# Optimization experiments

Hardware: AMD Instinct MI355X
Metric: run time of the kernel (lower is better)

The kernel has to match this reference:

```python
import jax, jax.numpy as jnp
import numpy as np

N, E, F, H, A, C, NC, L, AH = 50000, 800000, 768, 256, 128, 128, 7, 2, 4

def _ln(x, g, b):
    m = jnp.mean(x, axis=-1, keepdims=True)
    v = jnp.var(x, axis=-1, keepdims=True)
    return (x - m) / jnp.sqrt(v + 1e-5) * g + b

def setup_inputs() -> dict:
    key = jax.random.key(0)
    ks = jax.random.split(key, 32)
    s = 0.02
    d = {}
    d['x'] = jax.random.normal(ks[0], (N, F), jnp.float32)
    d['edge_index'] = jax.random.randint(ks[1], (2, E), 0, N, jnp.int32)
    d['W_in'] = jax.random.normal(ks[2], (F, H), jnp.float32) * s
    d['b_in'] = jnp.zeros((H,), jnp.float32)
    d['gin_W1'] = jax.random.normal(ks[3], (L, H, H), jnp.float32) * s
    d['gin_b1'] = jnp.zeros((L, H), jnp.float32)
    d['gin_lng'] = jnp.ones((L, H), jnp.float32)
    d['gin_lnb'] = jnp.zeros((L, H), jnp.float32)
    d['gin_W2'] = jax.random.normal(ks[4], (L, H, H), jnp.float32) * s
    d['gin_b2'] = jnp.zeros((L, H), jnp.float32)
    d['eps'] = jnp.zeros((L,), jnp.float32)
    d['ln_g'] = jnp.ones((L, H), jnp.float32)
    d['ln_b'] = jnp.zeros((L, H), jnp.float32)
    d['att_W1'] = jax.random.normal(ks[5], (AH, H, A), jnp.float32) * s
    d['att_b1'] = jnp.zeros((AH, A), jnp.float32)
    d['att_W2'] = jax.random.normal(ks[6], (AH, A), jnp.float32) * s
    d['att_b2'] = jnp.zeros((AH,), jnp.float32)
    d['Wc1'] = jax.random.normal(ks[7], (H, C), jnp.float32) * s
    d['bc1'] = jnp.zeros((C,), jnp.float32)
    d['lnc1_g'] = jnp.ones((C,), jnp.float32)
    d['lnc1_b'] = jnp.zeros((C,), jnp.float32)
    d['Wc2'] = jax.random.normal(ks[8], (C, C // 2), jnp.float32) * s
    d['bc2'] = jnp.zeros((C // 2,), jnp.float32)
    d['lnc2_g'] = jnp.ones((C // 2,), jnp.float32)
    d['lnc2_b'] = jnp.zeros((C // 2,), jnp.float32)
    d['Wc3'] = jax.random.normal(ks[9], (C // 2, NC), jnp.float32) * s
    d['bc3'] = jnp.zeros((NC,), jnp.float32)
    return d

def reference(x, edge_index, W_in, b_in, gin_W1, gin_b1, gin_lng, gin_lnb, gin_W2, gin_b2, eps, ln_g, ln_b, att_W1, att_b1, att_W2, att_b2, Wc1, bc1, lnc1_g, lnc1_b, Wc2, bc2, lnc2_g, lnc2_b, Wc3, bc3):
    src, dst = edge_index[0], edge_index[1]
    # input projection (use_residual and input_dim != gnn_hidden)
    h = x @ W_in + b_in  # [N,H]
    for i in range(L):
        agg = jax.ops.segment_sum(h[src], dst, num_segments=N)  # GIN sum aggregation
        m = (1.0 + eps[i]) * h + agg
        m = _ln(m @ gin_W1[i] + gin_b1[i], gin_lng[i], gin_lnb[i])
        m = jax.nn.relu(m) @ gin_W2[i] + gin_b2[i]
        hn = jax.nn.relu(_ln(m, ln_g[i], ln_b[i]))
        h = hn + h  # residual (shapes match)
    # multi-head attention pooling, softmax over node dim
    s = jnp.tanh(jnp.einsum('nd,kda->kna', h, att_W1) + att_b1[:, None, :])  # [AH,N,A]
    logits = jnp.einsum('kna,ka->kn', s, att_W2) + att_b2[:, None]  # [AH,N]
    a = jax.nn.softmax(logits, axis=1)  # [AH,N]
    z = jnp.einsum('kn,nd->kd', a, h)  # [AH,H]
    z_agg = jnp.mean(z, axis=0)  # [H]
    attn = a.T  # [N,AH]
    # classifier (full variant)
    c = jax.nn.relu(_ln(z_agg @ Wc1 + bc1, lnc1_g, lnc1_b))
    c = jax.nn.relu(_ln(c @ Wc2 + bc2, lnc2_g, lnc2_b))
    probs = jax.nn.softmax(c @ Wc3 + bc3, axis=0)
    return probs, attn
```

## Files before the change

kernel.cpp:

```cpp
#include <hip/hip_runtime.h>
#include <math.h>

#define NN 50000
#define NE 800000
#define FF 768
#define HH 256

typedef __attribute__((ext_vector_type(8))) short short8;
typedef __attribute__((ext_vector_type(4))) float f32x4;

__device__ inline unsigned short f2bf(float f) {
  unsigned u = __float_as_uint(f);
  u = u + 0x7fffu + ((u >> 16) & 1u);
  return (unsigned short)(u >> 16);
}
__device__ inline float bf2f(unsigned short b) {
  return __uint_as_float(((unsigned)b) << 16);
}

__device__ __forceinline__ void ldsload16(const unsigned short* g, unsigned short* l) {
  __builtin_amdgcn_global_load_lds(
      (const __attribute__((address_space(1))) void*)g,
      (__attribute__((address_space(3))) void*)l, 16, 0, 0);
}

__global__ void k_count(const int* __restrict__ dstv, int* __restrict__ deg) {
  int e = blockIdx.x * 256 + threadIdx.x;
  if (e < NE) atomicAdd(&deg[dstv[e]], 1);
}

__global__ void k_scan(const int* __restrict__ deg, int* __restrict__ rowptr) {
  const int CH = 49;
  int tid = threadIdx.x;
  int lane = tid & 63, w = tid >> 6;
  int base = tid * CH;
  int sum = 0;
  for (int i = 0; i < CH; i++) {
    int idx = base + i;
    if (idx < NN) sum += deg[idx];
  }
  int incl = sum;
  for (int off = 1; off < 64; off <<= 1) {
    int tv = __shfl_up(incl, off, 64);
    if (lane >= off) incl += tv;
  }
  __shared__ int ws[16];
  if (lane == 63) ws[w] = incl;
  __syncthreads();
  if (tid == 0) {
    int c = 0;
    for (int i = 0; i < 16; i++) { int tv = ws[i]; ws[i] = c; c += tv; }
  }
  __syncthreads();
  int run = ws[w] + (incl - sum);
  if (tid == 0) rowptr[0] = 0;
  for (int i = 0; i < CH; i++) {
    int idx = base + i;
    if (idx < NN) { run += deg[idx]; rowptr[idx + 1] = run; }
  }
}

__global__ void k_scatter(const int* __restrict__ srcv, const int* __restrict__ dstv,
                          int* __restrict__ cursor, int* __restrict__ csr_src) {
  int e = blockIdx.x * 256 + threadIdx.x;
  if (e < NE) {
    int d = dstv[e];
    int pos = atomicAdd(&cursor[d], 1);
    csr_src[pos] = srcv[e];
  }
}

__global__ void k_agg(const unsigned short* __restrict__ hb, const int* __restrict__ rowptr,
                      const int* __restrict__ csr_src, const float* __restrict__ eps,
                      int layer, unsigned short* __restrict__ mb) {
  int node = (blockIdx.x * blockDim.x + threadIdx.x) >> 6;
  int lane = threadIdx.x & 63;
  if (node >= NN) return;
  int beg = rowptr[node], end = rowptr[node + 1];
  const ushort4* hv = (const ushort4*)hb;
  float ax = 0.f, ay = 0.f, az = 0.f, aw = 0.f;
  for (int e = beg; e < end; ++e) {
    int s = csr_src[e];
    ushort4 v = hv[(size_t)s * 64 + lane];
    ax += bf2f(v.x); ay += bf2f(v.y); az += bf2f(v.z); aw += bf2f(v.w);
  }
  float ep = 1.0f + eps[layer];
  ushort4 h0 = hv[(size_t)node * 64 + lane];
  ax += ep * bf2f(h0.x); ay += ep * bf2f(h0.y);
  az += ep * bf2f(h0.z); aw += ep * bf2f(h0.w);
  ushort4 o;
  o.x = f2bf(ax); o.y = f2bf(ay); o.z = f2bf(az); o.w = f2bf(aw);
  *(ushort4*)&mb[(size_t)node * 256 + lane * 4] = o;
}

__global__ void k_tcast(const float* __restrict__ src0, unsigned short* __restrict__ dst0,
                        int R, int C) {
  const float* src = src0 + (size_t)blockIdx.z * R * C;
  unsigned short* dst = dst0 + (size_t)blockIdx.z * R * C;
  __shared__ float tile[32][33];
  int bx = blockIdx.x * 32, by = blockIdx.y * 32;
  int tx = threadIdx.x & 31, ty = threadIdx.x >> 5;
  for (int i = 0; i < 32; i += 8) {
    int r = by + ty + i, c = bx + tx;
    tile[ty + i][tx] = (r < R && c < C) ? src[(size_t)r * C + c] : 0.f;
  }
  __syncthreads();
  for (int i = 0; i < 32; i += 8) {
    int c = bx + ty + i, r = by + tx;
    if (c < C && r < R) dst[(size_t)c * R + r] = f2bf(tile[tx][ty + i]);
  }
}

__global__ __launch_bounds__(256) void k_mmff(
    const float* __restrict__ x, const unsigned short* __restrict__ Bt,
    const float* __restrict__ bias, float* __restrict__ outf,
    unsigned short* __restrict__ outb) {
  __shared__ unsigned short As[64 * 32];
  __shared__ unsigned short Bs[256 * 32];
  int t = threadIdx.x, lane = t & 63, wave = t >> 6;
  int row0 = blockIdx.x * 64;
  f32x4 acc[4][4];
#pragma unroll
  for (int i = 0; i < 4; i++)
#pragma unroll
    for (int j = 0; j < 4; j++) acc[i][j] = (f32x4)(0.f);
  int m16 = lane & 15, kq = lane >> 4;
  int arow = t >> 2, a2 = t & 3;
  int asl = a2 ^ (arow & 3);
  int agr = row0 + arow; if (agr >= NN) agr = NN - 1;
  int brow_[4], bsl_[4];
#pragma unroll
  for (int j = 0; j < 4; j++) {
    int s = j * 256 + t;
    brow_[j] = s >> 2;
    bsl_[j] = (s & 3) ^ (brow_[j] & 3);
  }
  for (int k0 = 0; k0 < FF; k0 += 32) {
    {
      const float* Af = x + (size_t)agr * FF + k0 + asl * 8;
      float4 f0 = *(const float4*)Af;
      float4 f1 = *(const float4*)(Af + 4);
      short8 v;
      v[0] = (short)f2bf(f0.x); v[1] = (short)f2bf(f0.y);
      v[2] = (short)f2bf(f0.z); v[3] = (short)f2bf(f0.w);
      v[4] = (short)f2bf(f1.x); v[5] = (short)f2bf(f1.y);
      v[6] = (short)f2bf(f1.z); v[7] = (short)f2bf(f1.w);
      *(short8*)&As[arow * 32 + a2 * 8] = v;
    }
#pragma unroll
    for (int j = 0; j < 4; j++)
      ldsload16(&Bt[(size_t)brow_[j] * FF + k0 + bsl_[j] * 8],
                &Bs[(j * 256 + wave * 64) * 8]);
    __syncthreads();
    short8 a[4], b[4];
#pragma unroll
    for (int rt = 0; rt < 4; rt++) {
      int row = rt * 16 + m16;
      a[rt] = *(const short8*)&As[row * 32 + ((kq ^ (row & 3)) * 8)];
    }
#pragma unroll
    for (int ct = 0; ct < 4; ct++) {
      int row = wave * 64 + ct * 16 + m16;
      b[ct] = *(const short8*)&Bs[row * 32 + ((kq ^ (row & 3)) * 8)];
    }
#pragma unroll
    for (int rt = 0; rt < 4; rt++)
#pragma unroll
      for (int ct = 0; ct < 4; ct++)
        acc[rt][ct] = __builtin_amdgcn_mfma_f32_16x16x32_bf16(a[rt], b[ct], acc[rt][ct], 0, 0, 0);
    __syncthreads();
  }
  int colbase = wave * 64 + m16;
  float bv[4];
#pragma unroll
  for (int ct = 0; ct < 4; ct++) bv[ct] = bias[colbase + ct * 16];
#pragma unroll
  for (int rt = 0; rt < 4; rt++)
#pragma unroll
    for (int reg = 0; reg < 4; reg++) {
      int r = row0 + rt * 16 + kq * 4 + reg;
      if (r < NN) {
#pragma unroll
        for (int ct = 0; ct < 4; ct++) {
          float v = acc[rt][ct][reg] + bv[ct];
          outf[(size_t)r * 256 + colbase + ct * 16] = v;
          outb[(size_t)r * 256 + colbase + ct * 16] = f2bf(v);
        }
      }
    }
}

template <bool WF>
__global__ __launch_bounds__(256) void k_gin(
    const unsigned short* __restrict__ Ab,
    const unsigned short* __restrict__ B1t, const float* __restrict__ bias1,
    const float* __restrict__ g1v, const float* __restrict__ be1,
    const unsigned short* __restrict__ B2t, const float* __restrict__ bias2,
    const float* __restrict__ g2v, const float* __restrict__ be2,
    const float* __restrict__ resid, float* __restrict__ outf,
    unsigned short* __restrict__ outb) {
  __shared__ unsigned short As[2][64 * 32];
  __shared__ unsigned short Bs[2][256 * 32];
  __shared__ unsigned short T1[64 * 256];
  __shared__ float redS[4][64];
  __shared__ float redQ[4][64];
  __shared__ float mvM[64], mvI[64];
  int t = threadIdx.x, lane = t & 63, wave = t >> 6;
  int row0 = blockIdx.x * 64;
  int m16 = lane & 15, kq = lane >> 4;
  int colbase = wave * 64 + m16;
  int arow = t >> 2, a2 = t & 3;
  int asl = a2 ^ (arow & 3);
  int agr = row0 + arow; if (agr >= NN) agr = NN - 1;
  const unsigned short* Ag = Ab + (size_t)agr * 256 + asl * 8;
  int brow_[4], bsl_[4];
#pragma unroll
  for (int j = 0; j < 4; j++) {
    int s = j * 256 + t;
    brow_[j] = s >> 2;
    bsl_[j] = (s & 3) ^ (brow_[j] & 3);
  }
  auto stage1 = [&](int c, int p) {
    int k0 = c * 32;
    ldsload16(Ag + k0, &As[p][wave * 512]);
#pragma unroll
    for (int j = 0; j < 4; j++)
      ldsload16(&B1t[(size_t)brow_[j] * 256 + k0 + bsl_[j] * 8],
                &Bs[p][(j * 256 + wave * 64) * 8]);
  };
  auto stage2 = [&](int c, int p) {
    int k0 = c * 32;
#pragma unroll
    for (int j = 0; j < 4; j++)
      ldsload16(&B2t[(size_t)brow_[j] * 256 + k0 + bsl_[j] * 8],
                &Bs[p][(j * 256 + wave * 64) * 8]);
  };

  f32x4 acc[4][4];
#pragma unroll
  for (int i = 0; i < 4; i++)
#pragma unroll
    for (int j = 0; j < 4; j++) acc[i][j] = (f32x4)(0.f);

  stage1(0, 0);
  stage1(1, 1);
#pragma unroll
  for (int c = 0; c < 8; c++) {
    if (c < 7) asm volatile("s_waitcnt vmcnt(5)" ::: "memory");
    else       asm volatile("s_waitcnt vmcnt(0)" ::: "memory");
    __builtin_amdgcn_s_barrier();
    asm volatile("" ::: "memory");
    const unsigned short* Ap = As[c & 1];
    const unsigned short* Bp = Bs[c & 1];
    short8 a[4], b[4];
#pragma unroll
    for (int rt = 0; rt < 4; rt++) {
      int row = rt * 16 + m16;
      a[rt] = *(const short8*)&Ap[row * 32 + ((kq ^ (row & 3)) * 8)];
    }
#pragma unroll
    for (int ct = 0; ct < 4; ct++) {
      int row = wave * 64 + ct * 16 + m16;
      b[ct] = *(const short8*)&Bp[row * 32 + ((kq ^ (row & 3)) * 8)];
    }
#pragma unroll
    for (int rt = 0; rt < 4; rt++)
#pragma unroll
      for (int ct = 0; ct < 4; ct++)
        acc[rt][ct] = __builtin_amdgcn_mfma_f32_16x16x32_bf16(a[rt], b[ct], acc[rt][ct], 0, 0, 0);
    asm volatile("" ::: "memory");
    __builtin_amdgcn_s_barrier();
    asm volatile("" ::: "memory");
    if (c + 2 < 8) stage1(c + 2, c & 1);
  }

  {
    float bv[4];
#pragma unroll
    for (int ct = 0; ct < 4; ct++) bv[ct] = bias1[colbase + ct * 16];
    float s[4][4], q[4][4];
#pragma unroll
    for (int rt = 0; rt < 4; rt++)
#pragma unroll
      for (int reg = 0; reg < 4; reg++) { s[rt][reg] = 0.f; q[rt][reg] = 0.f; }
#pragma unroll
    for (int rt = 0; rt < 4; rt++)
#pragma unroll
      for (int ct = 0; ct < 4; ct++)
#pragma unroll
        for (int reg = 0; reg < 4; reg++) {
          float v = acc[rt][ct][reg] + bv[ct];
          acc[rt][ct][reg] = v;
          s[rt][reg] += v;
          q[rt][reg] += v * v;
        }
#pragma unroll
    for (int off = 1; off < 16; off <<= 1) {
#pragma unroll
      for (int rt = 0; rt < 4; rt++)
#pragma unroll
        for (int reg = 0; reg < 4; reg++) {
          s[rt][reg] += __shfl_xor(s[rt][reg], off, 64);
          q[rt][reg] += __shfl_xor(q[rt][reg], off, 64);
        }
    }
    if (m16 == 0) {
#pragma unroll
      for (int rt = 0; rt < 4; rt++)
#pragma unroll
        for (int reg = 0; reg < 4; reg++) {
          redS[wave][rt * 16 + kq * 4 + reg] = s[rt][reg];
          redQ[wave][rt * 16 + kq * 4 + reg] = q[rt][reg];
        }
    }
    __syncthreads();
    if (t < 64) {
      float ss = redS[0][t] + redS[1][t] + redS[2][t] + redS[3][t];
      float qq = redQ[0][t] + redQ[1][t] + redQ[2][t] + redQ[3][t];
      float mean = ss * (1.f / 256.f);
      float var = qq * (1.f / 256.f) - mean * mean;
      mvM[t] = mean;
      mvI[t] = rsqrtf(var + 1e-5f);
    }
    __syncthreads();
    float gv[4], bev[4];
#pragma unroll
    for (int ct = 0; ct < 4; ct++) { gv[ct] = g1v[colbase + ct * 16]; bev[ct] = be1[colbase + ct * 16]; }
#pragma unroll
    for (int rt = 0; rt < 4; rt++)
#pragma unroll
      for (int reg = 0; reg < 4; reg++) {
        int rr = rt * 16 + kq * 4 + reg;
        float mean = mvM[rr], inv = mvI[rr];
#pragma unroll
        for (int ct = 0; ct < 4; ct++) {
          int col = colbase + ct * 16;
          float val = fmaxf((acc[rt][ct][reg] - mean) * inv * gv[ct] + bev[ct], 0.f);
          T1[rr * 256 + (((col >> 3) ^ (rr & 31)) * 8) + (col & 7)] = f2bf(val);
        }
      }
    __syncthreads();
  }

#pragma unroll
  for (int i = 0; i < 4; i++)
#pragma unroll
    for (int j = 0; j < 4; j++) acc[i][j] = (f32x4)(0.f);
  stage2(0, 0);
  stage2(1, 1);
#pragma unroll
  for (int c = 0; c < 8; c++) {
    if (c < 7) asm volatile("s_waitcnt vmcnt(4)" ::: "memory");
    else       asm volatile("s_waitcnt vmcnt(0)" ::: "memory");
    __builtin_amdgcn_s_barrier();
    asm volatile("" ::: "memory");
    const unsigned short* Bp = Bs[c & 1];
    short8 a[4], b[4];
#pragma unroll
    for (int rt = 0; rt < 4; rt++) {
      int row = rt * 16 + m16;
      int sl = (c * 4 + kq) ^ (row & 31);
      a[rt] = *(const short8*)&T1[row * 256 + sl * 8];
    }
#pragma unroll
    for (int ct = 0; ct < 4; ct++) {
      int row = wave * 64 + ct * 16 + m16;
      b[ct] = *(const short8*)&Bp[row * 32 + ((kq ^ (row & 3)) * 8)];
    }
#pragma unroll
    for (int rt = 0; rt < 4; rt++)
#pragma unroll
      for (int ct = 0; ct < 4; ct++)
        acc[rt][ct] = __builtin_amdgcn_mfma_f32_16x16x32_bf16(a[rt], b[ct], acc[rt][ct], 0, 0, 0);
    asm volatile("" ::: "memory");
    __builtin_amdgcn_s_barrier();
    asm volatile("" ::: "memory");
    if (c + 2 < 8) stage2(c + 2, c & 1);
  }

  {
    float bv[4];
#pragma unroll
    for (int ct = 0; ct < 4; ct++) bv[ct] = bias2[colbase + ct * 16];
    float s[4][4], q[4][4];
#pragma unroll
    for (int rt = 0; rt < 4; rt++)
#pragma unroll
      for (int reg = 0; reg < 4; reg++) { s[rt][reg] = 0.f; q[rt][reg] = 0.f; }
#pragma unroll
    for (int rt = 0; rt < 4; rt++)
#pragma unroll
      for (int ct = 0; ct < 4; ct++)
#pragma unroll
        for (int reg = 0; reg < 4; reg++) {
          float v = acc[rt][ct][reg] + bv[ct];
          acc[rt][ct][reg] = v;
          s[rt][reg] += v;
          q[rt][reg] += v * v;
        }
#pragma unroll
    for (int off = 1; off < 16; off <<= 1) {
#pragma unroll
      for (int rt = 0; rt < 4; rt++)
#pragma unroll
        for (int reg = 0; reg < 4; reg++) {
          s[rt][reg] += __shfl_xor(s[rt][reg], off, 64);
          q[rt][reg] += __shfl_xor(q[rt][reg], off, 64);
        }
    }
    if (m16 == 0) {
#pragma unroll
      for (int rt = 0; rt < 4; rt++)
#pragma unroll
        for (int reg = 0; reg < 4; reg++) {
          redS[wave][rt * 16 + kq * 4 + reg] = s[rt][reg];
          redQ[wave][rt * 16 + kq * 4 + reg] = q[rt][reg];
        }
    }
    __syncthreads();
    if (t < 64) {
      float ss = redS[0][t] + redS[1][t] + redS[2][t] + redS[3][t];
      float qq = redQ[0][t] + redQ[1][t] + redQ[2][t] + redQ[3][t];
      float mean = ss * (1.f / 256.f);
      float var = qq * (1.f / 256.f) - mean * mean;
      mvM[t] = mean;
      mvI[t] = rsqrtf(var + 1e-5f);
    }
    __syncthreads();
    float gv[4], bev[4];
#pragma unroll
    for (int ct = 0; ct < 4; ct++) { gv[ct] = g2v[colbase + ct * 16]; bev[ct] = be2[colbase + ct * 16]; }
#pragma unroll
    for (int rt = 0; rt < 4; rt++)
#pragma unroll
      for (int reg = 0; reg < 4; reg++) {
        int rr = rt * 16 + kq * 4 + reg;
        int r = row0 + rr;
        if (r >= NN) continue;
        float mean = mvM[rr], inv = mvI[rr];
#pragma unroll
        for (int ct = 0; ct < 4; ct++) {
          int col = colbase + ct * 16;
          float val = fmaxf((acc[rt][ct][reg] - mean) * inv * gv[ct] + bev[ct], 0.f);
          val += resid[(size_t)r * 256 + col];
          if (WF) outf[(size_t)r * 256 + col] = val;
          outb[(size_t)r * 256 + col] = f2bf(val);
        }
      }
  }
}

__global__ __launch_bounds__(256) void k_att(const unsigned short* __restrict__ hb,
    const unsigned short* __restrict__ W1T, const float* __restrict__ b1,
    const float* __restrict__ W2, const float* __restrict__ b2,
    float* __restrict__ logitsT) {
  __shared__ unsigned short As[64 * 32];
  __shared__ unsigned short Bs[512 * 32];
  int t = threadIdx.x, lane = t & 63, wave = t >> 6;
  int row0 = blockIdx.x * 64;
  f32x4 acc[4][8];
#pragma unroll
  for (int i = 0; i < 4; i++)
#pragma unroll
    for (int j = 0; j < 8; j++) acc[i][j] = (f32x4)(0.f);
  int m16 = lane & 15, kq = lane >> 4;
  int arow = t >> 2, a2 = t & 3;
  int asl = a2 ^ (arow & 3);
  int agr = row0 + arow; if (agr >= NN) agr = NN - 1;
  unsigned short* AsDst = &As[wave * 512];
  int brow_[8], bsl_[8];
#pragma unroll
  for (int j = 0; j < 8; j++) {
    int s = j * 256 + t;
    brow_[j] = s >> 2;
    bsl_[j] = (s & 3) ^ (brow_[j] & 3);
  }
  for (int k0 = 0; k0 < 256; k0 += 32) {
    ldsload16(&hb[(size_t)agr * 256 + k0 + asl * 8], AsDst);
#pragma unroll
    for (int j = 0; j < 8; j++)
      ldsload16(&W1T[(size_t)brow_[j] * 256 + k0 + bsl_[j] * 8],
                &Bs[(j * 256 + wave * 64) * 8]);
    __syncthreads();
    short8 a[4];
#pragma unroll
    for (int rt = 0; rt < 4; rt++) {
      int row = rt * 16 + m16;
      a[rt] = *(const short8*)&As[row * 32 + ((kq ^ (row & 3)) * 8)];
    }
#pragma unroll
    for (int ct = 0; ct < 8; ct++) {
      int row = wave * 128 + ct * 16 + m16;
      short8 b = *(const short8*)&Bs[row * 32 + ((kq ^ (row & 3)) * 8)];
#pragma unroll
      for (int rt = 0; rt < 4; rt++)
        acc[rt][ct] = __builtin_amdgcn_mfma_f32_16x16x32_bf16(a[rt], b, acc[rt][ct], 0, 0, 0);
    }
    __syncthreads();
  }
  const float* b1k = b1 + wave * 128;
  const float* w2k = W2 + wave * 128;
  float p[4][4];
#pragma unroll
  for (int rt = 0; rt < 4; rt++)
#pragma unroll
    for (int reg = 0; reg < 4; reg++) p[rt][reg] = 0.f;
#pragma unroll
  for (int ct = 0; ct < 8; ct++) {
    int col = ct * 16 + m16;
    float b1v = b1k[col], w2v = w2k[col];
#pragma unroll
    for (int rt = 0; rt < 4; rt++)
#pragma unroll
      for (int reg = 0; reg < 4; reg++) {
        float xv = acc[rt][ct][reg] + b1v;
        xv = fminf(fmaxf(xv, -10.f), 10.f);
        float ex = __expf(2.f * xv);
        p[rt][reg] += (ex - 1.f) / (ex + 1.f) * w2v;
      }
  }
#pragma unroll
  for (int off = 1; off < 16; off <<= 1)
#pragma unroll
    for (int rt = 0; rt < 4; rt++)
#pragma unroll
      for (int reg = 0; reg < 4; reg++) p[rt][reg] += __shfl_xor(p[rt][reg], off, 64);
  if (m16 == 0) {
    float b2v = b2[wave];
#pragma unroll
    for (int rt = 0; rt < 4; rt++)
#pragma unroll
      for (int reg = 0; reg < 4; reg++) {
        int r = row0 + rt * 16 + kq * 4 + reg;
        if (r < NN) logitsT[(size_t)wave * NN + r] = p[rt][reg] + b2v;
      }
  }
}

__global__ void k_smax1(const float* __restrict__ logitsT, float* __restrict__ pmax,
                        float* __restrict__ psum) {
  int k = blockIdx.y;
  int tid = threadIdx.x;
  const float* L = logitsT + (size_t)k * NN;
  __shared__ float sm[256];
  float mx = -1e30f;
  for (int i = blockIdx.x * 256 + tid; i < NN; i += 128 * 256) mx = fmaxf(mx, L[i]);
  sm[tid] = mx; __syncthreads();
  for (int o = 128; o >= 1; o >>= 1) { if (tid < o) sm[tid] = fmaxf(sm[tid], sm[tid + o]); __syncthreads(); }
  float bmax = sm[0];
  __syncthreads();
  float s = 0.f;
  for (int i = blockIdx.x * 256 + tid; i < NN; i += 128 * 256) s += __expf(L[i] - bmax);
  sm[tid] = s; __syncthreads();
  for (int o = 128; o >= 1; o >>= 1) { if (tid < o) sm[tid] += sm[tid + o]; __syncthreads(); }
  if (tid == 0) { pmax[k * 128 + blockIdx.x] = bmax; psum[k * 128 + blockIdx.x] = sm[0]; }
}

__global__ void k_smax2(const float* __restrict__ pmax, const float* __restrict__ psum,
                        float* __restrict__ gs) {
  int k = blockIdx.x;
  int tid = threadIdx.x;
  __shared__ float sm[128], sv[128];
  float m = pmax[k * 128 + tid];
  sm[tid] = m; __syncthreads();
  for (int o = 64; o >= 1; o >>= 1) { if (tid < o) sm[tid] = fmaxf(sm[tid], sm[tid + o]); __syncthreads(); }
  float gm = sm[0];
  __syncthreads();
  sv[tid] = psum[k * 128 + tid] * __expf(m - gm);
  __syncthreads();
  for (int o = 64; o >= 1; o >>= 1) { if (tid < o) sv[tid] += sv[tid + o]; __syncthreads(); }
  if (tid == 0) { gs[k * 2] = gm; gs[k * 2 + 1] = sv[0]; }
}

__global__ void k_attnz(const float* __restrict__ logitsT, const float* __restrict__ gs,
                        const unsigned short* __restrict__ hb, float* __restrict__ out_attn,
                        float* __restrict__ z) {
  int n0 = blockIdx.x * 128;
  int tid = threadIdx.x;
  __shared__ float a[4][128];
  for (int i = tid; i < 512; i += 256) {
    int k = i >> 7, n = i & 127;
    float v = 0.f;
    if (n0 + n < NN) v = __expf(logitsT[(size_t)k * NN + n0 + n] - gs[k * 2]) / gs[k * 2 + 1];
    a[k][n] = v;
  }
  __syncthreads();
  for (int i = tid; i < 512; i += 256) {
    int n = i >> 2, k = i & 3;
    if (n0 + n < NN) out_attn[(size_t)(n0 + n) * 4 + k] = a[k][n];
  }
  float z0 = 0.f, z1 = 0.f, z2 = 0.f, z3 = 0.f;
  int d = tid;
  int nmax = NN - n0; if (nmax > 128) nmax = 128;
  for (int n = 0; n < nmax; n++) {
    float hv = bf2f(hb[(size_t)(n0 + n) * 256 + d]);
    z0 += a[0][n] * hv; z1 += a[1][n] * hv; z2 += a[2][n] * hv; z3 += a[3][n] * hv;
  }
  atomicAdd(&z[0 * 256 + d], z0);
  atomicAdd(&z[1 * 256 + d], z1);
  atomicAdd(&z[2 * 256 + d], z2);
  atomicAdd(&z[3 * 256 + d], z3);
}

__global__ void k_cls(const float* __restrict__ z, const float* __restrict__ Wc1,
                      const float* __restrict__ bc1, const float* __restrict__ g1,
                      const float* __restrict__ b1, const float* __restrict__ Wc2,
                      const float* __restrict__ bc2, const float* __restrict__ g2,
                      const float* __restrict__ b2, const float* __restrict__ Wc3,
                      const float* __restrict__ bc3, float* __restrict__ out) {
  int tid = threadIdx.x;
  __shared__ float za[256];
  __shared__ float buf[256];
  __shared__ float c1s[128];
  __shared__ float c2s[64];
  za[tid] = 0.25f * (z[tid] + z[256 + tid] + z[512 + tid] + z[768 + tid]);
  __syncthreads();
  float v1 = 0.f;
  if (tid < 128) {
    for (int d = 0; d < 256; d++) v1 += za[d] * Wc1[d * 128 + tid];
    v1 += bc1[tid];
  }
  buf[tid] = (tid < 128) ? v1 : 0.f; __syncthreads();
  for (int o = 128; o >= 1; o >>= 1) { if (tid < o) buf[tid] += buf[tid + o]; __syncthreads(); }
  float mean1 = buf[0] * (1.f / 128.f);
  __syncthreads();
  buf[tid] = (tid < 128) ? (v1 - mean1) * (v1 - mean1) : 0.f; __syncthreads();
  for (int o = 128; o >= 1; o >>= 1) { if (tid < o) buf[tid] += buf[tid + o]; __syncthreads(); }
  float inv1 = rsqrtf(buf[0] * (1.f / 128.f) + 1e-5f);
  __syncthreads();
  if (tid < 128) c1s[tid] = fmaxf((v1 - mean1) * inv1 * g1[tid] + b1[tid], 0.f);
  __syncthreads();
  float v2 = 0.f;
  if (tid < 64) {
    for (int d = 0; d < 128; d++) v2 += c1s[d] * Wc2[d * 64 + tid];
    v2 += bc2[tid];
  }
  buf[tid] = (tid < 64) ? v2 : 0.f; __syncthreads();
  for (int o = 128; o >= 1; o >>= 1) { if (tid < o) buf[tid] += buf[tid + o]; __syncthreads(); }
  float mean2 = buf[0] * (1.f / 64.f);
  __syncthreads();
  buf[tid] = (tid < 64) ? (v2 - mean2) * (v2 - mean2) : 0.f; __syncthreads();
  for (int o = 128; o >= 1; o >>= 1) { if (tid < o) buf[tid] += buf[tid + o]; __syncthreads(); }
  float inv2 = rsqrtf(buf[0] * (1.f / 64.f) + 1e-5f);
  __syncthreads();
  if (tid < 64) c2s[tid] = fmaxf((v2 - mean2) * inv2 * g2[tid] + b2[tid], 0.f);
  __syncthreads();
  if (tid < 7) {
    float l = 0.f;
    for (int d = 0; d < 64; d++) l += c2s[d] * Wc3[d * 7 + tid];
    buf[tid] = l + bc3[tid];
  }
  __syncthreads();
  if (tid == 0) {
    float mx = -1e30f;
    for (int i = 0; i < 7; i++) mx = fmaxf(mx, buf[i]);
    float s = 0.f;
    for (int i = 0; i < 7; i++) s += __expf(buf[i] - mx);
    for (int i = 0; i < 7; i++) out[i] = __expf(buf[i] - mx) / s;
  }
}

extern "C" void kernel_launch(void* const* d_in, const int* in_sizes, int n_in,
                              void* d_out, int out_size, void* d_ws, size_t ws_size,
                              hipStream_t stream) {
  const float* x       = (const float*)d_in[0];
  const int*   ei      = (const int*)d_in[1];
  const float* W_in    = (const float*)d_in[2];
  const float* b_in    = (const float*)d_in[3];
  const float* gin_W1  = (const float*)d_in[4];
  const float* gin_b1  = (const float*)d_in[5];
  const float* gin_lng = (const float*)d_in[6];
  const float* gin_lnb = (const float*)d_in[7];
  const float* gin_W2  = (const float*)d_in[8];
  const float* gin_b2  = (const float*)d_in[9];
  const float* eps     = (const float*)d_in[10];
  const float* ln_g    = (const float*)d_in[11];
  const float* ln_b    = (const float*)d_in[12];
  const float* att_W1  = (const float*)d_in[13];
  const float* att_b1  = (const float*)d_in[14];
  const float* att_W2  = (const float*)d_in[15];
  const float* att_b2  = (const float*)d_in[16];
  const float* Wc1     = (const float*)d_in[17];
  const float* bc1     = (const float*)d_in[18];
  const float* lnc1_g  = (const float*)d_in[19];
  const float* lnc1_b  = (const float*)d_in[20];
  const float* Wc2     = (const float*)d_in[21];
  const float* bc2     = (const float*)d_in[22];
  const float* lnc2_g  = (const float*)d_in[23];
  const float* lnc2_b  = (const float*)d_in[24];
  const float* Wc3     = (const float*)d_in[25];
  const float* bc3     = (const float*)d_in[26];
  float* out = (float*)d_out;
  (void)in_sizes; (void)n_in; (void)out_size; (void)ws_size;

  char* wsb = (char*)d_ws;
  size_t off = 0;
  auto alloc = [&](size_t bytes) {
    char* p = wsb + off;
    off += (bytes + 255) & ~(size_t)255;
    return p;
  };
  float*          h       = (float*)alloc((size_t)NN * HH * 4);
  unsigned short* hb      = (unsigned short*)alloc((size_t)NN * HH * 2);
  unsigned short* mb1     = (unsigned short*)alloc((size_t)NN * HH * 2);
  unsigned short* WinT    = (unsigned short*)alloc((size_t)HH * FF * 2);
  unsigned short* g1T     = (unsigned short*)alloc((size_t)2 * HH * HH * 2);
  unsigned short* g2T     = (unsigned short*)alloc((size_t)2 * HH * HH * 2);
  unsigned short* aW1T    = (unsigned short*)alloc((size_t)4 * 128 * HH * 2);
  float*          logitsT = (float*)alloc((size_t)4 * NN * 4);
  int*            deg     = (int*)alloc((size_t)NN * 4);
  int*            rowptr  = (int*)alloc((size_t)(NN + 1) * 4);
  int*            cursor  = (int*)alloc((size_t)NN * 4);
  int*            csr_src = (int*)alloc((size_t)NE * 4);
  float*          pmax    = (float*)alloc(4 * 128 * 4);
  float*          psum    = (float*)alloc(4 * 128 * 4);
  float*          gs      = (float*)alloc(8 * 4);
  float*          z       = (float*)alloc(4 * 256 * 4);

  const int* srcv = ei;
  const int* dstv = ei + NE;

  k_tcast<<<dim3((HH + 31) / 32, (FF + 31) / 32, 1), 256, 0, stream>>>(W_in, WinT, FF, HH);
  k_tcast<<<dim3(8, 8, 2), 256, 0, stream>>>(gin_W1, g1T, HH, HH);
  k_tcast<<<dim3(8, 8, 2), 256, 0, stream>>>(gin_W2, g2T, HH, HH);
  k_tcast<<<dim3(4, 8, 4), 256, 0, stream>>>(att_W1, aW1T, HH, 128);

  hipMemsetAsync(deg, 0, (size_t)NN * 4, stream);
  hipMemsetAsync(z, 0, 4 * 256 * 4, stream);
  k_count<<<(NE + 255) / 256, 256, 0, stream>>>(dstv, deg);
  k_scan<<<1, 1024, 0, stream>>>(deg, rowptr);
  hipMemcpyAsync(cursor, rowptr, (size_t)NN * 4, hipMemcpyDeviceToDevice, stream);
  k_scatter<<<(NE + 255) / 256, 256, 0, stream>>>(srcv, dstv, cursor, csr_src);

  int gblocks = (NN + 63) / 64;
  k_mmff<<<gblocks, 256, 0, stream>>>(x, WinT, b_in, h, hb);

  for (int l = 0; l < 2; l++) {
    k_agg<<<(NN + 3) / 4, 256, 0, stream>>>(hb, rowptr, csr_src, eps, l, mb1);
    if (l == 0)
      k_gin<true><<<gblocks, 256, 0, stream>>>(
          mb1, g1T + (size_t)l * HH * HH, gin_b1 + l * HH, gin_lng + l * HH, gin_lnb + l * HH,
          g2T + (size_t)l * HH * HH, gin_b2 + l * HH, ln_g + l * HH, ln_b + l * HH,
          h, h, hb);
    else
      k_gin<false><<<gblocks, 256, 0, stream>>>(
          mb1, g1T + (size_t)l * HH * HH, gin_b1 + l * HH, gin_lng + l * HH, gin_lnb + l * HH,
          g2T + (size_t)l * HH * HH, gin_b2 + l * HH, ln_g + l * HH, ln_b + l * HH,
          h, nullptr, hb);
  }

  k_att<<<gblocks, 256, 0, stream>>>(hb, aW1T, att_b1, att_W2, att_b2, logitsT);
  k_smax1<<<dim3(128, 4), 256, 0, stream>>>(logitsT, pmax, psum);
  k_smax2<<<4, 128, 0, stream>>>(pmax, psum, gs);
  k_attnz<<<(NN + 127) / 128, 256, 0, stream>>>(logitsT, gs, hb, out + 7, z);
  k_cls<<<1, 256, 0, stream>>>(z, Wc1, bc1, lnc1_g, lnc1_b, Wc2, bc2, lnc2_g, lnc2_b,
                               Wc3, bc3, out);
}
```

Before: 904.8 us.

## Fuse attention-score projection into last GIN layer kernel and unroll aggregation

The separate attention kernel is removed. Its work now runs at the end of the second GIN kernel: the final bf16 hidden rows are written into the shared tile T1, and two MFMA passes over the attention weights compute the tanh·W2 logits, which are reduced per head via shared-memory atomics. This avoids re-reading the hidden state from global memory and saves a launch, but the GIN kernel gets longer and may use more registers. The aggregation loop is also unrolled by four to keep more gather loads in flight.

Measured after the change: 874.9 us. -3.3%, faster.

```diff
diff --git a/kernel.cpp b/kernel.cpp
--- a/kernel.cpp
+++ b/kernel.cpp
@@ -79,7 +79,19 @@
   int beg = rowptr[node], end = rowptr[node + 1];
   const ushort4* hv = (const ushort4*)hb;
   float ax = 0.f, ay = 0.f, az = 0.f, aw = 0.f;
-  for (int e = beg; e < end; ++e) {
+  int e = beg;
+  for (; e + 3 < end; e += 4) {
+    int s0 = csr_src[e], s1 = csr_src[e + 1], s2 = csr_src[e + 2], s3 = csr_src[e + 3];
+    ushort4 v0 = hv[(size_t)s0 * 64 + lane];
+    ushort4 v1 = hv[(size_t)s1 * 64 + lane];
+    ushort4 v2 = hv[(size_t)s2 * 64 + lane];
+    ushort4 v3 = hv[(size_t)s3 * 64 + lane];
+    ax += bf2f(v0.x) + bf2f(v1.x) + bf2f(v2.x) + bf2f(v3.x);
+    ay += bf2f(v0.y) + bf2f(v1.y) + bf2f(v2.y) + bf2f(v3.y);
+    az += bf2f(v0.z) + bf2f(v1.z) + bf2f(v2.z) + bf2f(v3.z);
+    aw += bf2f(v0.w) + bf2f(v1.w) + bf2f(v2.w) + bf2f(v3.w);
+  }
+  for (; e < end; ++e) {
     int s = csr_src[e];
     ushort4 v = hv[(size_t)s * 64 + lane];
     ax += bf2f(v.x); ay += bf2f(v.y); az += bf2f(v.z); aw += bf2f(v.w);
@@ -190,7 +202,7 @@
     }
 }
 
-template <bool WF>
+template <bool WF, bool ATT>
 __global__ __launch_bounds__(256) void k_gin(
     const unsigned short* __restrict__ Ab,
     const unsigned short* __restrict__ B1t, const float* __restrict__ bias1,
@@ -198,13 +210,17 @@
     const unsigned short* __restrict__ B2t, const float* __restrict__ bias2,
     const float* __restrict__ g2v, const float* __restrict__ be2,
     const float* __restrict__ resid, float* __restrict__ outf,
-    unsigned short* __restrict__ outb) {
+    unsigned short* __restrict__ outb,
+    const unsigned short* __restrict__ aW1T, const float* __restrict__ ab1,
+    const float* __restrict__ aW2v, const float* __restrict__ ab2,
+    float* __restrict__ logitsT) {
   __shared__ unsigned short As[2][64 * 32];
   __shared__ unsigned short Bs[2][256 * 32];
   __shared__ unsigned short T1[64 * 256];
   __shared__ float redS[4][64];
   __shared__ float redQ[4][64];
   __shared__ float mvM[64], mvI[64];
+  __shared__ float lg[4][64];
   int t = threadIdx.x, lane = t & 63, wave = t >> 6;
   int row0 = blockIdx.x * 64;
   int m16 = lane & 15, kq = lane >> 4;
@@ -228,11 +244,11 @@
       ldsload16(&B1t[(size_t)brow_[j] * 256 + k0 + bsl_[j] * 8],
                 &Bs[p][(j * 256 + wave * 64) * 8]);
   };
-  auto stage2 = [&](int c, int p) {
+  auto stageB = [&](const unsigned short* Bp_, int c, int p) {
     int k0 = c * 32;
 #pragma unroll
     for (int j = 0; j < 4; j++)
-      ldsload16(&B2t[(size_t)brow_[j] * 256 + k0 + bsl_[j] * 8],
+      ldsload16(&Bp_[(size_t)brow_[j] * 256 + k0 + bsl_[j] * 8],
                 &Bs[p][(j * 256 + wave * 64) * 8]);
   };
 
@@ -346,8 +362,8 @@
   for (int i = 0; i < 4; i++)
 #pragma unroll
     for (int j = 0; j < 4; j++) acc[i][j] = (f32x4)(0.f);
-  stage2(0, 0);
-  stage2(1, 1);
+  stageB(B2t, 0, 0);
+  stageB(B2t, 1, 1);
 #pragma unroll
   for (int c = 0; c < 8; c++) {
     if (c < 7) asm volatile("s_waitcnt vmcnt(4)" ::: "memory");
@@ -375,7 +391,7 @@
     asm volatile("" ::: "memory");
     __builtin_amdgcn_s_barrier();
     asm volatile("" ::: "memory");
-    if (c + 2 < 8) stage2(c + 2, c & 1);
+    if (c + 2 < 8) stageB(B2t, c + 2, c & 1);
   }
 
   {
@@ -445,95 +461,92 @@
           val += resid[(size_t)r * 256 + col];
           if (WF) outf[(size_t)r * 256 + col] = val;
           outb[(size_t)r * 256 + col] = f2bf(val);
+          if (ATT) T1[rr * 256 + (((col >> 3) ^ (rr & 31)) * 8) + (col & 7)] = f2bf(val);
         }
       }
   }
-}
-
-__global__ __launch_bounds__(256) void k_att(const unsigned short* __restrict__ hb,
-    const unsigned short* __restrict__ W1T, const float* __restrict__ b1,
-    const float* __restrict__ W2, const float* __restrict__ b2,
-    float* __restrict__ logitsT) {
-  __shared__ unsigned short As[64 * 32];
-  __shared__ unsigned short Bs[512 * 32];
-  int t = threadIdx.x, lane = t & 63, wave = t >> 6;
-  int row0 = blockIdx.x * 64;
-  f32x4 acc[4][8];
-#pragma unroll
-  for (int i = 0; i < 4; i++)
-#pragma unroll
-    for (int j = 0; j < 8; j++) acc[i][j] = (f32x4)(0.f);
-  int m16 = lane & 15, kq = lane >> 4;
-  int arow = t >> 2, a2 = t & 3;
-  int asl = a2 ^ (arow & 3);
-  int agr = row0 + arow; if (agr >= NN) agr = NN - 1;
-  unsigned short* AsDst = &As[wave * 512];
-  int brow_[8], bsl_[8];
-#pragma unroll
-  for (int j = 0; j < 8; j++) {
-    int s = j * 256 + t;
-    brow_[j] = s >> 2;
-    bsl_[j] = (s & 3) ^ (brow_[j] & 3);
-  }
-  for (int k0 = 0; k0 < 256; k0 += 32) {
-    ldsload16(&hb[(size_t)agr * 256 + k0 + asl * 8], AsDst);
-#pragma unroll
-    for (int j = 0; j < 8; j++)
-      ldsload16(&W1T[(size_t)brow_[j] * 256 + k0 + bsl_[j] * 8],
-                &Bs[(j * 256 + wave * 64) * 8]);
-    __syncthreads();
-    short8 a[4];
-#pragma unroll
-    for (int rt = 0; rt < 4; rt++) {
-      int row = rt * 16 + m16;
-      a[rt] = *(const short8*)&As[row * 32 + ((kq ^ (row & 3)) * 8)];
-    }
-#pragma unroll
-    for (int ct = 0; ct < 8; ct++) {
-      int row = wave * 128 + ct * 16 + m16;
-      short8 b = *(const short8*)&Bs[row * 32 + ((kq ^ (row & 3)) * 8)];
+
+  if (ATT) {
+    ((float*)lg)[t] = 0.f;
+    __syncthreads();
+#pragma unroll
+    for (int pass = 0; pass < 2; pass++) {
+#pragma unroll
+      for (int i = 0; i < 4; i++)
+#pragma unroll
+        for (int j = 0; j < 4; j++) acc[i][j] = (f32x4)(0.f);
+      const unsigned short* Wp = aW1T + (size_t)pass * 256 * 256;
+      stageB(Wp, 0, 0);
+      stageB(Wp, 1, 1);
+#pragma unroll
+      for (int c = 0; c < 8; c++) {
+        if (c < 7) asm volatile("s_waitcnt vmcnt(4)" ::: "memory");
+        else       asm volatile("s_waitcnt vmcnt(0)" ::: "memory");
+        __builtin_amdgcn_s_barrier();
+        asm volatile("" ::: "memory");
+        const unsigned short* Bp = Bs[c & 1];
+        short8 a[4], b[4];
+#pragma unroll
+        for (int rt = 0; rt < 4; rt++) {
+          int row = rt * 16 + m16;
+          int sl = (c * 4 + kq) ^ (row & 31);
+          a[rt] = *(const short8*)&T1[row * 256 + sl * 8];
+        }
+#pragma unroll
+        for (int ct = 0; ct < 4; ct++) {
+          int row = wave * 64 + ct * 16 + m16;
+          b[ct] = *(const short8*)&Bp[row * 32 + ((kq ^ (row & 3)) * 8)];
+        }
+#pragma unroll
+        for (int rt = 0; rt < 4; rt++)
+#pragma unroll
+          for (int ct = 0; ct < 4; ct++)
+            acc[rt][ct] = __builtin_amdgcn_mfma_f32_16x16x32_bf16(a[rt], b[ct], acc[rt][ct], 0, 0, 0);
+        asm volatile("" ::: "memory");
+        __builtin_amdgcn_s_barrier();
+        asm volatile("" ::: "memory");
+        if (c + 2 < 8) stageB(Wp, c + 2, c & 1);
+      }
+      int head = pass * 2 + (wave >> 1);
+      const float* b1k = ab1 + head * 128;
+      const float* w2k = aW2v + head * 128;
+      float p[4][4];
 #pragma unroll
       for (int rt = 0; rt < 4; rt++)
-        acc[rt][ct] = __builtin_amdgcn_mfma_f32_16x16x32_bf16(a[rt], b, acc[rt][ct], 0, 0, 0);
-    }
-    __syncthreads();
-  }
-  const float* b1k = b1 + wave * 128;
-  const float* w2k = W2 + wave * 128;
-  float p[4][4];
-#pragma unroll
-  for (int rt = 0; rt < 4; rt++)
-#pragma unroll
-    for (int reg = 0; reg < 4; reg++) p[rt][reg] = 0.f;
-#pragma unroll
-  for (int ct = 0; ct < 8; ct++) {
-    int col = ct * 16 + m16;
-    float b1v = b1k[col], w2v = w2k[col];
-#pragma unroll
-    for (int rt = 0; rt < 4; rt++)
-#pragma unroll
-      for (int reg = 0; reg < 4; reg++) {
-        float xv = acc[rt][ct][reg] + b1v;
-        xv = fminf(fmaxf(xv, -10.f), 10.f);
-        float ex = __expf(2.f * xv);
-        p[rt][reg] += (ex - 1.f) / (ex + 1.f) * w2v;
+#pragma unroll
+        for (int reg = 0; reg < 4; reg++) p[rt][reg] = 0.f;
+#pragma unroll
+      for (int ct = 0; ct < 4; ct++) {
+        int hcol = (wave & 1) * 64 + ct * 16 + m16;
+        float b1v = b1k[hcol], w2v = w2k[hcol];
+#pragma unroll
+        for (int rt = 0; rt < 4; rt++)
+#pragma unroll
+          for (int reg = 0; reg < 4; reg++) {
+            float xv = acc[rt][ct][reg] + b1v;
+            xv = fminf(fmaxf(xv, -10.f), 10.f);
+            float ex = __expf(2.f * xv);
+            p[rt][reg] += (ex - 1.f) / (ex + 1.f) * w2v;
+          }
       }
-  }
-#pragma unroll
-  for (int off = 1; off < 16; off <<= 1)
-#pragma unroll
-    for (int rt = 0; rt < 4; rt++)
-#pragma unroll
-      for (int reg = 0; reg < 4; reg++) p[rt][reg] += __shfl_xor(p[rt][reg], off, 64);
-  if (m16 == 0) {
-    float b2v = b2[wave];
-#pragma unroll
-    for (int rt = 0; rt < 4; rt++)
-#pragma unroll
-      for (int reg = 0; reg < 4; reg++) {
-        int r = row0 + rt * 16 + kq * 4 + reg;
-        if (r < NN) logitsT[(size_t)wave * NN + r] = p[rt][reg] + b2v;
+#pragma unroll
+      for (int off = 1; off < 16; off <<= 1)
+#pragma unroll
+        for (int rt = 0; rt < 4; rt++)
+#pragma unroll
+          for (int reg = 0; reg < 4; reg++) p[rt][reg] += __shfl_xor(p[rt][reg], off, 64);
+      if (m16 == 0) {
+#pragma unroll
+        for (int rt = 0; rt < 4; rt++)
+#pragma unroll
+          for (int reg = 0; reg < 4; reg++)
+            atomicAdd(&lg[head][rt * 16 + kq * 4 + reg], p[rt][reg]);
       }
+    }
+    __syncthreads();
+    int hh = t >> 6, rr2 = t & 63;
+    int r = row0 + rr2;
+    if (r < NN) logitsT[(size_t)hh * NN + r] = lg[hh][rr2] + ab2[hh];
   }
 }
 
@@ -738,18 +751,17 @@
   for (int l = 0; l < 2; l++) {
     k_agg<<<(NN + 3) / 4, 256, 0, stream>>>(hb, rowptr, csr_src, eps, l, mb1);
     if (l == 0)
-      k_gin<true><<<gblocks, 256, 0, stream>>>(
+      k_gin<true, false><<<gblocks, 256, 0, stream>>>(
           mb1, g1T + (size_t)l * HH * HH, gin_b1 + l * HH, gin_lng + l * HH, gin_lnb + l * HH,
           g2T + (size_t)l * HH * HH, gin_b2 + l * HH, ln_g + l * HH, ln_b + l * HH,
-          h, h, hb);
+          h, h, hb, nullptr, nullptr, nullptr, nullptr, nullptr);
     else
-      k_gin<false><<<gblocks, 256, 0, stream>>>(
+      k_gin<false, true><<<gblocks, 256, 0, stream>>>(
           mb1, g1T + (size_t)l * HH * HH, gin_b1 + l * HH, gin_lng + l * HH, gin_lnb + l * HH,
           g2T + (size_t)l * HH * HH, gin_b2 + l * HH, ln_g + l * HH, ln_b + l * HH,
-          h, nullptr, hb);
-  }
-
-  k_att<<<gblocks, 256, 0, stream>>>(hb, aW1T, att_b1, att_W2, att_b2, logitsT);
+          h, nullptr, hb, aW1T, att_b1, att_W2, att_b2, logitsT);
+  }
+
   k_smax1<<<dim3(128, 4), 256, 0, stream>>>(logitsT, pmax, psum);
   k_smax2<<<4, 128, 0, stream>>>(pmax, psum, gs);
   k_attnz<<<(NN + 127) / 128, 256, 0, stream>>>(logitsT, gs, hb, out + 7, z);
```
